# Performance work log

Hardware: AMD Instinct MI355X
Metric: run time of the kernel (lower is better)

The kernel has to match this reference:

```python
import jax, jax.numpy as jnp
import numpy as np

B, T, C, H = 16, 2048, 768, 128

def setup_inputs() -> dict:
    key = jax.random.key(0)
    k1, k2, k3, k4 = jax.random.split(key, 4)
    x = jax.random.normal(k1, (B, T, C), dtype=jnp.float32)
    Wq = jax.random.normal(k2, (C, H), dtype=jnp.float32) * (C ** -0.5)
    Wk = jax.random.normal(k3, (C, H), dtype=jnp.float32) * (C ** -0.5)
    Wv = jax.random.normal(k4, (C, H), dtype=jnp.float32) * (C ** -0.5)
    return {"x": x, "Wq": Wq, "Wk": Wk, "Wv": Wv}

def reference(x, Wq, Wk, Wv):
    Bc, Tc, Cc = x.shape
    q = jnp.einsum('btc,ch->bth', x, Wq)
    k = jnp.einsum('btc,ch->bth', x, Wk)
    v = jnp.einsum('btc,ch->bth', x, Wv)
    wei = jnp.einsum('bqh,bkh->bqk', q, k)  # [B,T,T]
    tril = jnp.tril(jnp.ones((Tc, Tc), dtype=jnp.float32))
    # Faithful to original: mask with -inf FIRST, then scale by C**-0.5
    wei = jnp.where(tril == 0, -jnp.inf, wei) * (Cc ** -0.5)
    wei = jax.nn.softmax(wei, axis=-1)
    out = jnp.einsum('bqk,bkh->bqh', wei, v)
    return out
```

## Files before the change

kernel.cpp:

```cpp
#include <hip/hip_runtime.h>
#include <hip/hip_bf16.h>
#include <cstdint>

#define B_ 16
#define T_ 2048
#define C_ 768
#define H_ 128

typedef __bf16 bf16x8 __attribute__((ext_vector_type(8)));
typedef float f32x4 __attribute__((ext_vector_type(4)));
typedef unsigned short u16x8 __attribute__((ext_vector_type(8)));

__device__ __forceinline__ void gld_lds16(const void* g, void* s) {
    __builtin_amdgcn_global_load_lds(
        (__attribute__((address_space(1))) void*)(size_t)g,
        (__attribute__((address_space(3))) void*)s,
        16, 0, 0);
}

__device__ __forceinline__ unsigned short f2bf(float f) {
    __bf16 h = (__bf16)f;
    return __builtin_bit_cast(unsigned short, h);
}

__global__ __launch_bounds__(256) void wxconv_kernel(
    const float* __restrict__ Wq, const float* __restrict__ Wk,
    const float* __restrict__ Wv, const float* __restrict__ x,
    unsigned short* __restrict__ wT, unsigned short* __restrict__ xb) {
    int bidx = blockIdx.x;
    if (bidx < 1152) {
        int idx = bidx * 256 + threadIdx.x;
        if (idx >= 3 * H_ * C_) return;
        int w = idx / (H_ * C_);
        int r = idx % (H_ * C_);
        int h = r / C_;
        int c = r % C_;
        const float* W = (w == 0) ? Wq : ((w == 1) ? Wk : Wv);
        wT[idx] = f2bf(W[c * H_ + h]);
    } else {
        size_t i = ((size_t)(bidx - 1152) * 256 + threadIdx.x) * 8;
        f32x4 a = *(const f32x4*)(x + i);
        f32x4 b = *(const f32x4*)(x + i + 4);
        u16x8 o;
        o[0] = f2bf(a[0]); o[1] = f2bf(a[1]); o[2] = f2bf(a[2]); o[3] = f2bf(a[3]);
        o[4] = f2bf(b[0]); o[5] = f2bf(b[1]); o[6] = f2bf(b[2]); o[7] = f2bf(b[3]);
        *(u16x8*)(xb + i) = o;
    }
}

__global__ __launch_bounds__(256) void proj_bf16_kernel(
    const unsigned short* __restrict__ xb, const unsigned short* __restrict__ wT,
    unsigned short* __restrict__ qb, unsigned short* __restrict__ kb,
    unsigned short* __restrict__ vtb) {
    __shared__ unsigned short Asm[128 * 64];
    __shared__ unsigned short Bsm[128 * 64];

    const int tid = threadIdx.x;
    const int w = blockIdx.x % 3;
    const int mt = blockIdx.x / 3;
    const int m0 = mt * 128;
    const unsigned short* wTw = wT + (size_t)w * (H_ * C_);

    const int wid = tid >> 6;
    const int lane = tid & 63;
    const int wm = (wid >> 1) * 64;
    const int wn = (wid & 1) * 64;
    const int quad = lane >> 4;
    const int lo16 = lane & 15;

    f32x4 acc[4][4] = {};

    for (int kt = 0; kt < 12; ++kt) {
        const int k0 = kt * 64;
        __syncthreads();
#pragma unroll
        for (int j = 0; j < 4; ++j) {
            int cidx = j * 256 + tid;
            int m = cidx >> 3;
            int c = (cidx & 7) ^ (m & 7);
            gld_lds16((const char*)xb + ((size_t)(m0 + m) * C_ + k0 + c * 8) * 2,
                      (char*)Asm + (j * 256 + wid * 64) * 16);
        }
#pragma unroll
        for (int j = 0; j < 4; ++j) {
            int cidx = j * 256 + tid;
            int n = cidx >> 3;
            int c = (cidx & 7) ^ (n & 7);
            gld_lds16((const char*)wTw + ((size_t)n * C_ + k0 + c * 8) * 2,
                      (char*)Bsm + (j * 256 + wid * 64) * 16);
        }
        __syncthreads();

#pragma unroll
        for (int kk = 0; kk < 2; ++kk) {
            bf16x8 afrag[4], bfrag[4];
#pragma unroll
            for (int mi = 0; mi < 4; ++mi) {
                int m = wm + mi * 16 + lo16;
                int c = (kk * 4 + quad) ^ (m & 7);
                afrag[mi] = *(const bf16x8*)((const __bf16*)Asm + m * 64 + c * 8);
            }
#pragma unroll
            for (int ni = 0; ni < 4; ++ni) {
                int n = wn + ni * 16 + lo16;
                int c = (kk * 4 + quad) ^ (n & 7);
                bfrag[ni] = *(const bf16x8*)((const __bf16*)Bsm + n * 64 + c * 8);
            }
#pragma unroll
            for (int mi = 0; mi < 4; ++mi)
#pragma unroll
                for (int ni = 0; ni < 4; ++ni)
                    acc[mi][ni] = __builtin_amdgcn_mfma_f32_16x16x32_bf16(
                        afrag[mi], bfrag[ni], acc[mi][ni], 0, 0, 0);
        }
    }

    if (w < 2) {
        unsigned short* out = (w == 0) ? qb : kb;
#pragma unroll
        for (int mi = 0; mi < 4; ++mi) {
            int rowb = m0 + wm + mi * 16 + quad * 4;
#pragma unroll
            for (int ni = 0; ni < 4; ++ni) {
                int col = wn + ni * 16 + lo16;
#pragma unroll
                for (int r = 0; r < 4; ++r)
                    out[(size_t)(rowb + r) * H_ + col] = f2bf(acc[mi][ni][r]);
            }
        }
    } else {
        int b = m0 >> 11;
        int t0 = (m0 & 2047) + wm;
#pragma unroll
        for (int mi = 0; mi < 4; ++mi) {
            int t = t0 + mi * 16 + quad * 4;
#pragma unroll
            for (int ni = 0; ni < 4; ++ni) {
                int col = wn + ni * 16 + lo16;
                ushort4 pk;
                pk.x = f2bf(acc[mi][ni][0]); pk.y = f2bf(acc[mi][ni][1]);
                pk.z = f2bf(acc[mi][ni][2]); pk.w = f2bf(acc[mi][ni][3]);
                *(ushort4*)(vtb + ((size_t)b * H_ + col) * T_ + t) = pk;
            }
        }
    }
}

__global__ __launch_bounds__(256, 2) void attn_kernel(
    const unsigned short* __restrict__ qb, const unsigned short* __restrict__ kb,
    const unsigned short* __restrict__ vtb, float* __restrict__ out) {
    __shared__ unsigned short Ks[128 * 128];
    __shared__ unsigned short Vs[128 * 128];
    __shared__ unsigned short Ps[4][16 * 72];

    const int tid = threadIdx.x;
    const int bid = blockIdx.x;
    const int b = bid & 15;
    const int i = bid >> 4;
    const int qt = (i < 16) ? (31 - i) : (i - 16);
    const int q0 = qt * 64;

    const unsigned short* qB = qb + (size_t)b * T_ * H_;
    const unsigned short* kB = kb + (size_t)b * T_ * H_;
    const unsigned short* vB = vtb + (size_t)b * H_ * T_;

    const int wid = tid >> 6;
    const int lane = tid & 63;
    const int quad = lane >> 4;
    const int lo16 = lane & 15;

    bf16x8 qfrag[4];
    {
        const unsigned short* qrow = qB + (size_t)(q0 + wid * 16 + lo16) * H_ + quad * 8;
#pragma unroll
        for (int ks = 0; ks < 4; ++ks)
            qfrag[ks] = *(const bf16x8*)(qrow + ks * 32);
    }

    float l_part = 0.f;
    f32x4 oacc[8] = {};
    const float cs = 0.05205877694341f;
    unsigned short* Pw = &Ps[wid][0];

    const int nst = (qt + 2) >> 1;
    for (int jt = 0; jt < nst; ++jt) {
        const int kv0s = jt * 128;
        __syncthreads();
#pragma unroll
        for (int rnd = 0; rnd < 8; ++rnd) {
            int cidx = rnd * 256 + tid;
            int m = cidx >> 4;
            int c = (cidx & 15) ^ (m & 15);
            gld_lds16((const char*)kB + ((size_t)(kv0s + m) * H_ + c * 8) * 2,
                      (char*)Ks + (rnd * 256 + wid * 64) * 16);
        }
#pragma unroll
        for (int rnd = 0; rnd < 8; ++rnd) {
            int cidx = rnd * 256 + tid;
            int d = cidx >> 4;
            int c = (cidx & 15) ^ (d & 15);
            gld_lds16((const char*)vB + ((size_t)d * T_ + kv0s + c * 8) * 2,
                      (char*)Vs + (rnd * 256 + wid * 64) * 16);
        }
        __syncthreads();

        for (int hh = 0; hh < 2 && kv0s + hh * 64 <= q0; ++hh) {
            f32x4 s[4] = {};
#pragma unroll
            for (int ks = 0; ks < 4; ++ks) {
#pragma unroll
                for (int ni = 0; ni < 4; ++ni) {
                    int row = hh * 64 + ni * 16 + lo16;
                    int slot = (ks * 4 + quad) ^ lo16;
                    bf16x8 kf = *(const bf16x8*)((const __bf16*)Ks + row * 128 + slot * 8);
                    s[ni] = __builtin_amdgcn_mfma_f32_16x16x32_bf16(kf, qfrag[ks], s[ni], 0, 0, 0);
                }
            }

            const bool diag = (kv0s + hh * 64 == q0);
            if (diag) {
#pragma unroll
                for (int ni = 0; ni < 4; ++ni) {
#pragma unroll
                    for (int r = 0; r < 4; ++r) {
                        float p = exp2f(s[ni][r] * cs);
                        if (ni * 16 + quad * 4 + r > wid * 16 + lo16) p = 0.f;
                        l_part += p;
                        s[ni][r] = p;
                    }
                    ushort4 w4;
                    w4.x = f2bf(s[ni][0]); w4.y = f2bf(s[ni][1]);
                    w4.z = f2bf(s[ni][2]); w4.w = f2bf(s[ni][3]);
                    *(ushort4*)(Pw + lo16 * 72 + ni * 16 + quad * 4) = w4;
                }
            } else {
#pragma unroll
                for (int ni = 0; ni < 4; ++ni) {
#pragma unroll
                    for (int r = 0; r < 4; ++r) {
                        float p = exp2f(s[ni][r] * cs);
                        l_part += p;
                        s[ni][r] = p;
                    }
                    ushort4 w4;
                    w4.x = f2bf(s[ni][0]); w4.y = f2bf(s[ni][1]);
                    w4.z = f2bf(s[ni][2]); w4.w = f2bf(s[ni][3]);
                    *(ushort4*)(Pw + lo16 * 72 + ni * 16 + quad * 4) = w4;
                }
            }

#pragma unroll
            for (int ks2 = 0; ks2 < 2; ++ks2) {
                bf16x8 pf = *(const bf16x8*)((const __bf16*)Pw + lo16 * 72 + ks2 * 32 + quad * 8);
#pragma unroll
                for (int nd = 0; nd < 8; ++nd) {
                    int dn = nd * 16 + lo16;
                    int slot = (hh * 8 + ks2 * 4 + quad) ^ lo16;
                    bf16x8 vf = *(const bf16x8*)((const __bf16*)Vs + dn * 128 + slot * 8);
                    oacc[nd] = __builtin_amdgcn_mfma_f32_16x16x32_bf16(pf, vf, oacc[nd], 0, 0, 0);
                }
            }
        }
    }

    l_part += __shfl_xor(l_part, 16);
    l_part += __shfl_xor(l_part, 32);
#pragma unroll
    for (int r = 0; r < 4; ++r) {
        float lv = __shfl(l_part, quad * 4 + r);
        float inv = 1.0f / lv;
        int qrow = q0 + wid * 16 + quad * 4 + r;
        float* orow = out + ((size_t)b * T_ + qrow) * H_;
#pragma unroll
        for (int nd = 0; nd < 8; ++nd)
            orow[nd * 16 + lo16] = oacc[nd][r] * inv;
    }
}

extern "C" void kernel_launch(void* const* d_in, const int* in_sizes, int n_in,
                              void* d_out, int out_size, void* d_ws, size_t ws_size,
                              hipStream_t stream) {
    const float* x = (const float*)d_in[0];
    const float* Wq = (const float*)d_in[1];
    const float* Wk = (const float*)d_in[2];
    const float* Wv = (const float*)d_in[3];
    float* out = (float*)d_out;

    char* ws = (char*)d_ws;
    unsigned short* wT  = (unsigned short*)ws;
    unsigned short* qb  = (unsigned short*)(ws + (1ull << 20));
    unsigned short* kb  = (unsigned short*)(ws + (9ull << 20));
    unsigned short* vtb = (unsigned short*)(ws + (17ull << 20));
    unsigned short* xb  = (unsigned short*)(ws + (25ull << 20));

    hipLaunchKernelGGL(wxconv_kernel, dim3(13440), dim3(256), 0, stream, Wq, Wk, Wv, x, wT, xb);
    hipLaunchKernelGGL(proj_bf16_kernel, dim3(768), dim3(256), 0, stream, xb, wT, qb, kb, vtb);
    hipLaunchKernelGGL(attn_kernel, dim3(512), dim3(256), 0, stream, qb, kb, vtb, out);
}
```

Before: 231.7 us.

## Split causal attention into balanced halves with partial combine; fuse QKV projection

The projection kernel now computes Q, K and V together per 64-row tile, loading one x tile against all three weight matrices. This improves reuse of x from shared memory. Attention is rebalanced: each block pair handles a short query tile plus half of a long tile's KV range, with 64-wide KV steps. Partial unnormalized outputs and row sums go to workspace, and a new combine kernel merges them. This adds an extra launch and global traffic for the partial results in exchange for even per-block work.

Result: faster. 221.6 us (-4.3%).

```diff
diff --git a/kernel.cpp b/kernel.cpp
--- a/kernel.cpp
+++ b/kernel.cpp
@@ -48,60 +48,55 @@
     }
 }
 
-__global__ __launch_bounds__(256) void proj_bf16_kernel(
+__global__ __launch_bounds__(256, 2) void proj_kernel(
     const unsigned short* __restrict__ xb, const unsigned short* __restrict__ wT,
     unsigned short* __restrict__ qb, unsigned short* __restrict__ kb,
     unsigned short* __restrict__ vtb) {
-    __shared__ unsigned short Asm[128 * 64];
-    __shared__ unsigned short Bsm[128 * 64];
+    __shared__ unsigned short Asm[64 * 64];
+    __shared__ unsigned short Bsm[384 * 64];
 
     const int tid = threadIdx.x;
-    const int w = blockIdx.x % 3;
-    const int mt = blockIdx.x / 3;
-    const int m0 = mt * 128;
-    const unsigned short* wTw = wT + (size_t)w * (H_ * C_);
-
+    const int m0 = blockIdx.x * 64;
     const int wid = tid >> 6;
     const int lane = tid & 63;
-    const int wm = (wid >> 1) * 64;
-    const int wn = (wid & 1) * 64;
     const int quad = lane >> 4;
     const int lo16 = lane & 15;
-
-    f32x4 acc[4][4] = {};
+    const int wn = wid * 96;
+
+    f32x4 acc[4][6] = {};
 
     for (int kt = 0; kt < 12; ++kt) {
         const int k0 = kt * 64;
         __syncthreads();
 #pragma unroll
-        for (int j = 0; j < 4; ++j) {
-            int cidx = j * 256 + tid;
+        for (int rnd = 0; rnd < 2; ++rnd) {
+            int cidx = rnd * 256 + tid;
             int m = cidx >> 3;
             int c = (cidx & 7) ^ (m & 7);
             gld_lds16((const char*)xb + ((size_t)(m0 + m) * C_ + k0 + c * 8) * 2,
-                      (char*)Asm + (j * 256 + wid * 64) * 16);
-        }
-#pragma unroll
-        for (int j = 0; j < 4; ++j) {
-            int cidx = j * 256 + tid;
+                      (char*)Asm + (rnd * 256 + wid * 64) * 16);
+        }
+#pragma unroll
+        for (int rnd = 0; rnd < 12; ++rnd) {
+            int cidx = rnd * 256 + tid;
             int n = cidx >> 3;
             int c = (cidx & 7) ^ (n & 7);
-            gld_lds16((const char*)wTw + ((size_t)n * C_ + k0 + c * 8) * 2,
-                      (char*)Bsm + (j * 256 + wid * 64) * 16);
+            gld_lds16((const char*)wT + ((size_t)(n >> 7) * (H_ * C_) + (n & 127) * C_ + k0 + c * 8) * 2,
+                      (char*)Bsm + (rnd * 256 + wid * 64) * 16);
         }
         __syncthreads();
 
 #pragma unroll
         for (int kk = 0; kk < 2; ++kk) {
-            bf16x8 afrag[4], bfrag[4];
+            bf16x8 afrag[4], bfrag[6];
 #pragma unroll
             for (int mi = 0; mi < 4; ++mi) {
-                int m = wm + mi * 16 + lo16;
+                int m = mi * 16 + lo16;
                 int c = (kk * 4 + quad) ^ (m & 7);
                 afrag[mi] = *(const bf16x8*)((const __bf16*)Asm + m * 64 + c * 8);
             }
 #pragma unroll
-            for (int ni = 0; ni < 4; ++ni) {
+            for (int ni = 0; ni < 6; ++ni) {
                 int n = wn + ni * 16 + lo16;
                 int c = (kk * 4 + quad) ^ (n & 7);
                 bfrag[ni] = *(const bf16x8*)((const __bf16*)Bsm + n * 64 + c * 8);
@@ -109,34 +104,28 @@
 #pragma unroll
             for (int mi = 0; mi < 4; ++mi)
 #pragma unroll
-                for (int ni = 0; ni < 4; ++ni)
+                for (int ni = 0; ni < 6; ++ni)
                     acc[mi][ni] = __builtin_amdgcn_mfma_f32_16x16x32_bf16(
                         afrag[mi], bfrag[ni], acc[mi][ni], 0, 0, 0);
         }
     }
 
-    if (w < 2) {
-        unsigned short* out = (w == 0) ? qb : kb;
-#pragma unroll
-        for (int mi = 0; mi < 4; ++mi) {
-            int rowb = m0 + wm + mi * 16 + quad * 4;
-#pragma unroll
-            for (int ni = 0; ni < 4; ++ni) {
-                int col = wn + ni * 16 + lo16;
-#pragma unroll
-                for (int r = 0; r < 4; ++r)
-                    out[(size_t)(rowb + r) * H_ + col] = f2bf(acc[mi][ni][r]);
-            }
-        }
-    } else {
-        int b = m0 >> 11;
-        int t0 = (m0 & 2047) + wm;
-#pragma unroll
-        for (int mi = 0; mi < 4; ++mi) {
-            int t = t0 + mi * 16 + quad * 4;
-#pragma unroll
-            for (int ni = 0; ni < 4; ++ni) {
-                int col = wn + ni * 16 + lo16;
+#pragma unroll
+    for (int mi = 0; mi < 4; ++mi) {
+        int grow = m0 + mi * 16 + quad * 4;
+#pragma unroll
+        for (int ni = 0; ni < 6; ++ni) {
+            int n = wn + ni * 16 + lo16;
+            int wmat = n >> 7;
+            int col = n & 127;
+            if (wmat < 2) {
+                unsigned short* o = (wmat == 0) ? qb : kb;
+#pragma unroll
+                for (int rr = 0; rr < 4; ++rr)
+                    o[(size_t)(grow + rr) * H_ + col] = f2bf(acc[mi][ni][rr]);
+            } else {
+                int b = grow >> 11;
+                int t = grow & 2047;
                 ushort4 pk;
                 pk.x = f2bf(acc[mi][ni][0]); pk.y = f2bf(acc[mi][ni][1]);
                 pk.z = f2bf(acc[mi][ni][2]); pk.w = f2bf(acc[mi][ni][3]);
@@ -146,19 +135,112 @@
     }
 }
 
+__device__ __forceinline__ void attn_seg(
+    const unsigned short* kB, const unsigned short* vB, const bf16x8 qfrag[4],
+    int j0, int j1, int jmask, float& l_part, f32x4 oacc[8],
+    unsigned short* Ks, unsigned short* Vs, unsigned short* Pw,
+    int tid, int wid, int quad, int lo16) {
+    const float cs = 0.05205877694341f;
+    for (int j = j0; j < j1; ++j) {
+        const int kv0 = j * 64;
+        __syncthreads();
+#pragma unroll
+        for (int rnd = 0; rnd < 4; ++rnd) {
+            int cidx = rnd * 256 + tid;
+            int m = cidx >> 4;
+            int c = (cidx & 15) ^ (m & 15);
+            gld_lds16((const char*)kB + ((size_t)(kv0 + m) * H_ + c * 8) * 2,
+                      (char*)Ks + (rnd * 256 + wid * 64) * 16);
+        }
+#pragma unroll
+        for (int rnd = 0; rnd < 4; ++rnd) {
+            int cidx = rnd * 256 + tid;
+            int d = cidx >> 3;
+            int c = (cidx & 7) ^ (d & 7);
+            gld_lds16((const char*)vB + ((size_t)d * T_ + kv0 + c * 8) * 2,
+                      (char*)Vs + (rnd * 256 + wid * 64) * 16);
+        }
+        __syncthreads();
+
+        f32x4 s[4] = {};
+#pragma unroll
+        for (int ks = 0; ks < 4; ++ks) {
+#pragma unroll
+            for (int ni = 0; ni < 4; ++ni) {
+                int row = ni * 16 + lo16;
+                int slot = (ks * 4 + quad) ^ lo16;
+                bf16x8 kf = *(const bf16x8*)((const __bf16*)Ks + row * 128 + slot * 8);
+                s[ni] = __builtin_amdgcn_mfma_f32_16x16x32_bf16(kf, qfrag[ks], s[ni], 0, 0, 0);
+            }
+        }
+
+        const bool diag = (j == jmask);
+        if (diag) {
+#pragma unroll
+            for (int ni = 0; ni < 4; ++ni) {
+#pragma unroll
+                for (int rr = 0; rr < 4; ++rr) {
+                    float p = exp2f(s[ni][rr] * cs);
+                    if (ni * 16 + quad * 4 + rr > wid * 16 + lo16) p = 0.f;
+                    l_part += p;
+                    s[ni][rr] = p;
+                }
+                ushort4 w4;
+                w4.x = f2bf(s[ni][0]); w4.y = f2bf(s[ni][1]);
+                w4.z = f2bf(s[ni][2]); w4.w = f2bf(s[ni][3]);
+                *(ushort4*)(Pw + lo16 * 72 + ni * 16 + quad * 4) = w4;
+            }
+        } else {
+#pragma unroll
+            for (int ni = 0; ni < 4; ++ni) {
+#pragma unroll
+                for (int rr = 0; rr < 4; ++rr) {
+                    float p = exp2f(s[ni][rr] * cs);
+                    l_part += p;
+                    s[ni][rr] = p;
+                }
+                ushort4 w4;
+                w4.x = f2bf(s[ni][0]); w4.y = f2bf(s[ni][1]);
+                w4.z = f2bf(s[ni][2]); w4.w = f2bf(s[ni][3]);
+                *(ushort4*)(Pw + lo16 * 72 + ni * 16 + quad * 4) = w4;
+            }
+        }
+
+#pragma unroll
+        for (int ks2 = 0; ks2 < 2; ++ks2) {
+            bf16x8 pf = *(const bf16x8*)((const __bf16*)Pw + lo16 * 72 + ks2 * 32 + quad * 8);
+#pragma unroll
+            for (int nd = 0; nd < 8; ++nd) {
+                int dn = nd * 16 + lo16;
+                int vc = (ks2 * 4 + quad) ^ (dn & 7);
+                bf16x8 vf = *(const bf16x8*)((const __bf16*)Vs + dn * 64 + vc * 8);
+                oacc[nd] = __builtin_amdgcn_mfma_f32_16x16x32_bf16(pf, vf, oacc[nd], 0, 0, 0);
+            }
+        }
+    }
+}
+
+__device__ __forceinline__ void load_qfrag(const unsigned short* qB, int q0,
+                                           int wid, int quad, int lo16, bf16x8 qf[4]) {
+    const unsigned short* qrow = qB + (size_t)(q0 + wid * 16 + lo16) * H_ + quad * 8;
+#pragma unroll
+    for (int ks = 0; ks < 4; ++ks) qf[ks] = *(const bf16x8*)(qrow + ks * 32);
+}
+
 __global__ __launch_bounds__(256, 2) void attn_kernel(
     const unsigned short* __restrict__ qb, const unsigned short* __restrict__ kb,
-    const unsigned short* __restrict__ vtb, float* __restrict__ out) {
-    __shared__ unsigned short Ks[128 * 128];
-    __shared__ unsigned short Vs[128 * 128];
+    const unsigned short* __restrict__ vtb, float* __restrict__ out,
+    float* __restrict__ pO, float* __restrict__ pL) {
+    __shared__ unsigned short Ks[64 * 128];
+    __shared__ unsigned short Vs[128 * 64];
     __shared__ unsigned short Ps[4][16 * 72];
 
     const int tid = threadIdx.x;
     const int bid = blockIdx.x;
-    const int b = bid & 15;
-    const int i = bid >> 4;
-    const int qt = (i < 16) ? (31 - i) : (i - 16);
-    const int q0 = qt * 64;
+    const int half = bid >> 8;
+    const int slot = bid & 255;
+    const int r = slot >> 4;
+    const int b = slot & 15;
 
     const unsigned short* qB = qb + (size_t)b * T_ * H_;
     const unsigned short* kB = kb + (size_t)b * T_ * H_;
@@ -168,112 +250,75 @@
     const int lane = tid & 63;
     const int quad = lane >> 4;
     const int lo16 = lane & 15;
-
-    bf16x8 qfrag[4];
-    {
-        const unsigned short* qrow = qB + (size_t)(q0 + wid * 16 + lo16) * H_ + quad * 8;
-#pragma unroll
-        for (int ks = 0; ks < 4; ++ks)
-            qfrag[ks] = *(const bf16x8*)(qrow + ks * 32);
-    }
-
+    unsigned short* Pw = &Ps[wid][0];
+
+    const int qtb = 31 - r;
+    bf16x8 qf[4];
     float l_part = 0.f;
     f32x4 oacc[8] = {};
-    const float cs = 0.05205877694341f;
-    unsigned short* Pw = &Ps[wid][0];
-
-    const int nst = (qt + 2) >> 1;
-    for (int jt = 0; jt < nst; ++jt) {
-        const int kv0s = jt * 128;
-        __syncthreads();
-#pragma unroll
-        for (int rnd = 0; rnd < 8; ++rnd) {
-            int cidx = rnd * 256 + tid;
-            int m = cidx >> 4;
-            int c = (cidx & 15) ^ (m & 15);
-            gld_lds16((const char*)kB + ((size_t)(kv0s + m) * H_ + c * 8) * 2,
-                      (char*)Ks + (rnd * 256 + wid * 64) * 16);
-        }
-#pragma unroll
-        for (int rnd = 0; rnd < 8; ++rnd) {
-            int cidx = rnd * 256 + tid;
-            int d = cidx >> 4;
-            int c = (cidx & 15) ^ (d & 15);
-            gld_lds16((const char*)vB + ((size_t)d * T_ + kv0s + c * 8) * 2,
-                      (char*)Vs + (rnd * 256 + wid * 64) * 16);
-        }
-        __syncthreads();
-
-        for (int hh = 0; hh < 2 && kv0s + hh * 64 <= q0; ++hh) {
-            f32x4 s[4] = {};
-#pragma unroll
-            for (int ks = 0; ks < 4; ++ks) {
-#pragma unroll
-                for (int ni = 0; ni < 4; ++ni) {
-                    int row = hh * 64 + ni * 16 + lo16;
-                    int slot = (ks * 4 + quad) ^ lo16;
-                    bf16x8 kf = *(const bf16x8*)((const __bf16*)Ks + row * 128 + slot * 8);
-                    s[ni] = __builtin_amdgcn_mfma_f32_16x16x32_bf16(kf, qfrag[ks], s[ni], 0, 0, 0);
-                }
-            }
-
-            const bool diag = (kv0s + hh * 64 == q0);
-            if (diag) {
-#pragma unroll
-                for (int ni = 0; ni < 4; ++ni) {
-#pragma unroll
-                    for (int r = 0; r < 4; ++r) {
-                        float p = exp2f(s[ni][r] * cs);
-                        if (ni * 16 + quad * 4 + r > wid * 16 + lo16) p = 0.f;
-                        l_part += p;
-                        s[ni][r] = p;
-                    }
-                    ushort4 w4;
-                    w4.x = f2bf(s[ni][0]); w4.y = f2bf(s[ni][1]);
-                    w4.z = f2bf(s[ni][2]); w4.w = f2bf(s[ni][3]);
-                    *(ushort4*)(Pw + lo16 * 72 + ni * 16 + quad * 4) = w4;
-                }
-            } else {
-#pragma unroll
-                for (int ni = 0; ni < 4; ++ni) {
-#pragma unroll
-                    for (int r = 0; r < 4; ++r) {
-                        float p = exp2f(s[ni][r] * cs);
-                        l_part += p;
-                        s[ni][r] = p;
-                    }
-                    ushort4 w4;
-                    w4.x = f2bf(s[ni][0]); w4.y = f2bf(s[ni][1]);
-                    w4.z = f2bf(s[ni][2]); w4.w = f2bf(s[ni][3]);
-                    *(ushort4*)(Pw + lo16 * 72 + ni * 16 + quad * 4) = w4;
-                }
-            }
-
-#pragma unroll
-            for (int ks2 = 0; ks2 < 2; ++ks2) {
-                bf16x8 pf = *(const bf16x8*)((const __bf16*)Pw + lo16 * 72 + ks2 * 32 + quad * 8);
-#pragma unroll
-                for (int nd = 0; nd < 8; ++nd) {
-                    int dn = nd * 16 + lo16;
-                    int slot = (hh * 8 + ks2 * 4 + quad) ^ lo16;
-                    bf16x8 vf = *(const bf16x8*)((const __bf16*)Vs + dn * 128 + slot * 8);
-                    oacc[nd] = __builtin_amdgcn_mfma_f32_16x16x32_bf16(pf, vf, oacc[nd], 0, 0, 0);
-                }
-            }
-        }
+
+    if (half == 0) {
+        load_qfrag(qB, r * 64, wid, quad, lo16, qf);
+        attn_seg(kB, vB, qf, 0, r + 1, r, l_part, oacc, Ks, Vs, Pw, tid, wid, quad, lo16);
+        l_part += __shfl_xor(l_part, 16);
+        l_part += __shfl_xor(l_part, 32);
+#pragma unroll
+        for (int rr = 0; rr < 4; ++rr) {
+            float lv = __shfl(l_part, quad * 4 + rr);
+            float inv = 1.0f / lv;
+            int qrow = r * 64 + wid * 16 + quad * 4 + rr;
+            float* orow = out + ((size_t)b * T_ + qrow) * H_;
+#pragma unroll
+            for (int nd = 0; nd < 8; ++nd)
+                orow[nd * 16 + lo16] = oacc[nd][rr] * inv;
+        }
+        l_part = 0.f;
+#pragma unroll
+        for (int nd = 0; nd < 8; ++nd) oacc[nd] = f32x4{0.f, 0.f, 0.f, 0.f};
+        load_qfrag(qB, qtb * 64, wid, quad, lo16, qf);
+        attn_seg(kB, vB, qf, 0, 16 - r, -1, l_part, oacc, Ks, Vs, Pw, tid, wid, quad, lo16);
+    } else {
+        load_qfrag(qB, qtb * 64, wid, quad, lo16, qf);
+        attn_seg(kB, vB, qf, 16 - r, 32 - r, qtb, l_part, oacc, Ks, Vs, Pw, tid, wid, quad, lo16);
     }
 
     l_part += __shfl_xor(l_part, 16);
     l_part += __shfl_xor(l_part, 32);
-#pragma unroll
-    for (int r = 0; r < 4; ++r) {
-        float lv = __shfl(l_part, quad * 4 + r);
-        float inv = 1.0f / lv;
-        int qrow = q0 + wid * 16 + quad * 4 + r;
-        float* orow = out + ((size_t)b * T_ + qrow) * H_;
+    float* myO = pO + (size_t)(half * 256 + slot) * (64 * 128);
+    if (lane < 16) pL[(half * 256 + slot) * 64 + wid * 16 + lo16] = l_part;
+#pragma unroll
+    for (int rr = 0; rr < 4; ++rr) {
+        int ql = wid * 16 + quad * 4 + rr;
 #pragma unroll
         for (int nd = 0; nd < 8; ++nd)
-            orow[nd * 16 + lo16] = oacc[nd][r] * inv;
+            myO[ql * 128 + nd * 16 + lo16] = oacc[nd][rr];
+    }
+}
+
+__global__ __launch_bounds__(256) void combine_kernel(
+    const float* __restrict__ pO, const float* __restrict__ pL,
+    float* __restrict__ out) {
+    const int slot = blockIdx.x;
+    const int r = slot >> 4;
+    const int b = slot & 15;
+    const int q0 = (31 - r) * 64;
+    __shared__ float ls[64];
+    const int tid = threadIdx.x;
+    if (tid < 64) ls[tid] = pL[slot * 64 + tid] + pL[(256 + slot) * 64 + tid];
+    __syncthreads();
+    const float* O0 = pO + (size_t)slot * (64 * 128);
+    const float* O1 = pO + (size_t)(256 + slot) * (64 * 128);
+    float* ob = out + ((size_t)b * T_ + q0) * H_;
+#pragma unroll
+    for (int k = 0; k < 8; ++k) {
+        int idx = (k * 256 + tid) * 4;
+        f32x4 a = *(const f32x4*)(O0 + idx);
+        f32x4 c = *(const f32x4*)(O1 + idx);
+        float inv = 1.0f / ls[idx >> 7];
+        f32x4 o;
+        o[0] = (a[0] + c[0]) * inv; o[1] = (a[1] + c[1]) * inv;
+        o[2] = (a[2] + c[2]) * inv; o[3] = (a[3] + c[3]) * inv;
+        *(f32x4*)(ob + idx) = o;
     }
 }
 
@@ -292,8 +337,11 @@
     unsigned short* kb  = (unsigned short*)(ws + (9ull << 20));
     unsigned short* vtb = (unsigned short*)(ws + (17ull << 20));
     unsigned short* xb  = (unsigned short*)(ws + (25ull << 20));
+    float* pO = (float*)(ws + (80ull << 20));
+    float* pL = (float*)(ws + (100ull << 20));
 
     hipLaunchKernelGGL(wxconv_kernel, dim3(13440), dim3(256), 0, stream, Wq, Wk, Wv, x, wT, xb);
-    hipLaunchKernelGGL(proj_bf16_kernel, dim3(768), dim3(256), 0, stream, xb, wT, qb, kb, vtb);
-    hipLaunchKernelGGL(attn_kernel, dim3(512), dim3(256), 0, stream, qb, kb, vtb, out);
-}
+    hipLaunchKernelGGL(proj_kernel, dim3(512), dim3(256), 0, stream, xb, wT, qb, kb, vtb);
+    hipLaunchKernelGGL(attn_kernel, dim3(512), dim3(256), 0, stream, qb, kb, vtb, out, pO, pL);
+    hipLaunchKernelGGL(combine_kernel, dim3(256), dim3(256), 0, stream, pO, pL, out);
+}
```
